# Performance work log

Hardware: AMD Instinct MI355X
Metric: run time of the kernel (lower is better)

## Reference

```python
import jax, jax.numpy as jnp
import numpy as np
import math

B, T, C, D = 8, 2048, 1024, 1024
N_LAYER, LAYER_ID = 24, 12


def setup_inputs() -> dict:
    key = jax.random.key(0)
    ks = jax.random.split(key, 5)
    r01 = LAYER_ID / (N_LAYER - 1)
    r10 = 1.0 - LAYER_ID / N_LAYER
    ddd = np.arange(C, dtype=np.float64) / C                      # (C,)
    h = np.arange(D, dtype=np.float64)
    decay_speed = -5 + 8 * (h / (D - 1)) ** (0.7 + 1.3 * r01)     # time_decay init
    zigzag = ((np.arange(D) + 1) % 3 - 1) * 0.5
    time_first = np.log(0.3) + zigzag
    scale = C ** -0.5
    return {
        "x": jax.random.normal(ks[0], (B, T, C), jnp.float32),
        "time_decay": jnp.asarray(decay_speed, jnp.float32),
        "time_first": jnp.asarray(time_first, jnp.float32),
        "time_mix_k": jnp.asarray(ddd ** r10, jnp.float32),
        "time_mix_v": jnp.asarray(ddd ** r10 + 0.3 * r01, jnp.float32),
        "time_mix_r": jnp.asarray(ddd ** (0.5 * r10), jnp.float32),
        "Wk": jax.random.normal(ks[1], (D, C), jnp.float32) * scale,
        "Wv": jax.random.normal(ks[2], (D, C), jnp.float32) * scale,
        "Wr": jax.random.normal(ks[3], (D, C), jnp.float32) * scale,
        "Wo": jax.random.normal(ks[4], (C, D), jnp.float32) * scale,
    }


def _wkv(time_decay, time_first, k, v):
    # wkv_t = (e^{u+k_t} v_t + A_{t-1}) / (e^{u+k_t} + B_{t-1})
    # A_t = e^w A_{t-1} + e^{k_t} v_t ;  B_t likewise with v=1 ;  w = -exp(time_decay)
    # Exactly the math of the original conv1d-with-exp-curve trick, in O(T).
    ew = jnp.exp(-jnp.exp(time_decay))   # (D,)
    eu = jnp.exp(time_first)             # (D,)
    ek = jnp.exp(k)                      # [B,T,D]
    ekv = ek * v

    def step(carry, inp):
        a, b = carry                     # [B,D] each
        ekt, ekvt = inp                  # [B,D] each
        out = (eu * ekvt + a) / (eu * ekt + b)
        return (ew * a + ekvt, ew * b + ekt), out

    init = (jnp.zeros_like(ek[:, 0]), jnp.zeros_like(ek[:, 0]))
    xs = (jnp.swapaxes(ek, 0, 1), jnp.swapaxes(ekv, 0, 1))  # [T,B,D]
    _, out = jax.lax.scan(step, init, xs)
    return jnp.swapaxes(out, 0, 1)       # [B,T,D]


def reference(x, time_decay, time_first, time_mix_k, time_mix_v, time_mix_r, Wk, Wv, Wr, Wo):
    # time_shift: prepend zero row, drop last (ZeroPad2d((0,0,1,-1)))
    xx = jnp.pad(x, ((0, 0), (1, 0), (0, 0)))[:, :-1]
    xk = x * time_mix_k + xx * (1 - time_mix_k)
    xv = x * time_mix_v + xx * (1 - time_mix_v)
    xr = x * time_mix_r + xx * (1 - time_mix_r)
    k = jnp.einsum('btc,dc->btd', xk, Wk)
    v = jnp.einsum('btc,dc->btd', xv, Wv)
    sr = jax.nn.sigmoid(jnp.einsum('btc,dc->btd', xr, Wr))
    rwkv = sr * _wkv(time_decay, time_first, k, v)
    return jnp.einsum('btd,cd->btc', rwkv, Wo)
```

## Files before the change

### kernel.cpp

```cpp
#include <hip/hip_runtime.h>
#include <cstdint>
#include <cstddef>

#define Bb 8
#define Tt 2048
#define Cc 1024
#define Dd 1024
#define Mm (Bb*Tt)
#define CL 64
#define NCH (Tt/CL)


typedef __bf16  bf16x8  __attribute__((ext_vector_type(8)));
typedef float   floatx4 __attribute__((ext_vector_type(4)));

#define MFMA16(a, b, c) __builtin_amdgcn_mfma_f32_16x16x32_bf16((a), (b), (c), 0, 0, 0)

__device__ __forceinline__ ushort f2bf(float f) {
    unsigned u = __float_as_uint(f);
    u = (u + 0x7FFF + ((u >> 16) & 1)) >> 16;
    return (ushort)u;
}
__device__ __forceinline__ float bf2f(ushort u) {
    return __uint_as_float(((unsigned)u) << 16);
}

__device__ __forceinline__ void load_lds16(const void* g, void* l) {
    __builtin_amdgcn_global_load_lds((__attribute__((address_space(1))) void*)(g),
                                     (__attribute__((address_space(3))) void*)(l),
                                     16, 0, 0);
}

#define CFENCE asm volatile("" ::: "memory")
#define BARRIER do { CFENCE; __builtin_amdgcn_s_barrier(); CFENCE; } while (0)

__global__ __launch_bounds__(256) void prep_mix3(
        const float* __restrict__ x,
        const float* __restrict__ mk, const float* __restrict__ mv,
        const float* __restrict__ mr,
        ushort* __restrict__ xk, ushort* __restrict__ xv, ushort* __restrict__ xr) {
    int i  = blockIdx.x * 256 + threadIdx.x;
    int cq = i & (Cc / 8 - 1);
    int m  = i >> 7;
    int t  = m & (Tt - 1);
    float xc[8], xp[8];
    *(float4*)&xc[0] = ((const float4*)x)[i * 2];
    *(float4*)&xc[4] = ((const float4*)x)[i * 2 + 1];
    if (t != 0) {
        *(float4*)&xp[0] = ((const float4*)x)[(i - Cc / 8) * 2];
        *(float4*)&xp[4] = ((const float4*)x)[(i - Cc / 8) * 2 + 1];
    } else {
#pragma unroll
        for (int j = 0; j < 8; j++) xp[j] = 0.f;
    }
    float wk[8], wv[8], wr[8];
    *(float4*)&wk[0] = ((const float4*)mk)[cq * 2];
    *(float4*)&wk[4] = ((const float4*)mk)[cq * 2 + 1];
    *(float4*)&wv[0] = ((const float4*)mv)[cq * 2];
    *(float4*)&wv[4] = ((const float4*)mv)[cq * 2 + 1];
    *(float4*)&wr[0] = ((const float4*)mr)[cq * 2];
    *(float4*)&wr[4] = ((const float4*)mr)[cq * 2 + 1];
    ushort ok[8], ov[8], orr[8];
#pragma unroll
    for (int j = 0; j < 8; j++) {
        float d = xc[j] - xp[j];
        ok[j]  = f2bf(xp[j] + d * wk[j]);
        ov[j]  = f2bf(xp[j] + d * wv[j]);
        orr[j] = f2bf(xp[j] + d * wr[j]);
    }
    ((ulonglong2*)xk)[i] = *(const ulonglong2*)ok;
    ((ulonglong2*)xv)[i] = *(const ulonglong2*)ov;
    ((ulonglong2*)xr)[i] = *(const ulonglong2*)orr;
}

__global__ __launch_bounds__(256) void cvt_w(
        const float* __restrict__ wk, const float* __restrict__ wv,
        const float* __restrict__ wr, const float* __restrict__ wo,
        ushort* __restrict__ ok, ushort* __restrict__ ov,
        ushort* __restrict__ orr, ushort* __restrict__ oo) {
    int i = blockIdx.x * 256 + threadIdx.x;
    int sel = i >> 18;
    int j = i & ((1 << 18) - 1);
    const float* s = sel == 0 ? wk : sel == 1 ? wv : sel == 2 ? wr : wo;
    ushort* d      = sel == 0 ? ok : sel == 1 ? ov : sel == 2 ? orr : oo;
    float4 f = ((const float4*)s)[j];
    ushort4 o;
    o.x = f2bf(f.x); o.y = f2bf(f.y); o.z = f2bf(f.z); o.w = f2bf(f.w);
    ((ushort4*)d)[j] = o;
}

struct Gemm9 {
    floatx4 acc[8][4];
    int quad, fr, wm, wn;

    __device__ __forceinline__ void run(
            const ushort* __restrict__ A, const ushort* __restrict__ Bw,
            long tm, long tn, int Kdim, __bf16* LDSb) {
        const int tid  = threadIdx.x;
        const int lane = tid & 63;
        quad = lane >> 4;
        fr   = lane & 15;
        const int wave = tid >> 6;
        wm = (wave >> 2) * 128;
        wn = (wave & 3) * 64;
        const int x7 = fr & 7;
        const int g0 = (quad ^ x7) * 8;
        const int g1 = ((4 + quad) ^ x7) * 8;

        const int srow = tid >> 3;
        const int scol = ((tid & 7) ^ (srow & 7)) * 8;
        const int wlds = wave * 512;
        const ushort* Ag[4];
#pragma unroll
        for (int j = 0; j < 4; j++)
            Ag[j] = A + (tm + j * 64 + srow) * (long)Kdim + scol;

        auto stageA = [&](int buf, long koff) {
            __bf16* d = LDSb + buf * 16384;
#pragma unroll
            for (int j = 0; j < 4; j++)
                load_lds16(Ag[j] + koff, d + j * 4096 + wlds);
        };

        const ushort* Bq[4];
#pragma unroll
        for (int ni = 0; ni < 4; ni++)
            Bq[ni] = Bw + (tn + wn + ni * 16 + fr) * (long)Kdim + quad * 8;

        floatx4 zero = {0.f, 0.f, 0.f, 0.f};
#pragma unroll
        for (int ai = 0; ai < 8; ai++)
#pragma unroll
            for (int nj = 0; nj < 4; nj++) acc[ai][nj] = zero;

        const int NT = Kdim >> 6;

        stageA(0, 0);
        CFENCE;
        if (NT > 1) stageA(1, 64);
        bf16x8 b0[4], b1[4], bn0[4];
#pragma unroll
        for (int ni = 0; ni < 4; ni++) b0[ni] = *(const bf16x8*)(Bq[ni]);
#pragma unroll
        for (int ni = 0; ni < 4; ni++) b1[ni] = *(const bf16x8*)(Bq[ni] + 32);
        asm volatile("s_waitcnt vmcnt(12)" ::: "memory");
        BARRIER;

        int bc = 0, bs = 2;
        for (int T = 0; T < NT; ++T) {
            const __bf16* Ab = LDSb + bc * 16384;
            const long knext = (long)(T + 1) * 64;
            if (T + 1 < NT) {
#pragma unroll
                for (int ni = 0; ni < 4; ni++)
                    bn0[ni] = *(const bf16x8*)(Bq[ni] + knext);
            }
            if (T + 2 < NT)
                stageA(bs, (long)(T + 2) * 64);

            bf16x8 a0[4], a1[4];
#pragma unroll
            for (int r = 0; r < 4; r++)
                a0[r] = *(const bf16x8*)&Ab[(wm + r * 16 + fr) * 64 + g0];
#pragma unroll
            for (int r = 0; r < 4; r++)
                a1[r] = *(const bf16x8*)&Ab[(wm + 64 + r * 16 + fr) * 64 + g0];
            __builtin_amdgcn_s_setprio(1);
#pragma unroll
            for (int r = 0; r < 4; r++)
#pragma unroll
                for (int ni = 0; ni < 4; ni++)
                    acc[r][ni] = MFMA16(a0[r], b0[ni], acc[r][ni]);
#pragma unroll
            for (int r = 0; r < 4; r++)
#pragma unroll
                for (int ni = 0; ni < 4; ni++)
                    acc[4 + r][ni] = MFMA16(a1[r], b0[ni], acc[4 + r][ni]);
            __builtin_amdgcn_s_setprio(0);
#pragma unroll
            for (int r = 0; r < 4; r++)
                a0[r] = *(const bf16x8*)&Ab[(wm + r * 16 + fr) * 64 + g1];
#pragma unroll
            for (int r = 0; r < 4; r++)
                a1[r] = *(const bf16x8*)&Ab[(wm + 64 + r * 16 + fr) * 64 + g1];
            __builtin_amdgcn_s_setprio(1);
#pragma unroll
            for (int r = 0; r < 4; r++)
#pragma unroll
                for (int ni = 0; ni < 4; ni++)
                    acc[r][ni] = MFMA16(a0[r], b1[ni], acc[r][ni]);
#pragma unroll
            for (int r = 0; r < 4; r++)
#pragma unroll
                for (int ni = 0; ni < 4; ni++)
                    acc[4 + r][ni] = MFMA16(a1[r], b1[ni], acc[4 + r][ni]);
            __builtin_amdgcn_s_setprio(0);

            if (T + 1 < NT) {
#pragma unroll
                for (int ni = 0; ni < 4; ni++)
                    b1[ni] = *(const bf16x8*)(Bq[ni] + knext + 32);
#pragma unroll
                for (int ni = 0; ni < 4; ni++) b0[ni] = bn0[ni];
                asm volatile("s_waitcnt vmcnt(8)" ::: "memory");
                BARRIER;
            }
            if (++bc == 3) bc = 0;
            if (++bs == 3) bs = 0;
        }
    }
};

template<int MODE>
__global__ __launch_bounds__(512, 2) void gemm_nt(
        const ushort* __restrict__ A, const ushort* __restrict__ Bw,
        void* __restrict__ Co, int Ndim, int Kdim) {
    __shared__ __attribute__((aligned(16))) __bf16 LDSb[3 * 16384];
    const int orig = blockIdx.y * 64 + blockIdx.x;
    const int L    = (orig & 7) * 32 + (orig >> 3);
    const long tm = (long)(L >> 2) * 256;
    const long tn = (long)(L & 3) * 256;
    Gemm9 g;
    g.run(A, Bw, tm, tn, Kdim, LDSb);
#pragma unroll
    for (int ai = 0; ai < 8; ai++)
#pragma unroll
        for (int nj = 0; nj < 4; nj++)
#pragma unroll
            for (int r = 0; r < 4; r++) {
                long grow = tm + g.wm + ai * 16 + g.quad * 4 + r;
                long gcol = tn + g.wn + nj * 16 + g.fr;
                float v = g.acc[ai][nj][r];
                if (MODE == 2) v = 1.f / (1.f + __expf(-v));
                if (MODE == 0)      ((float*)Co)[grow * Ndim + gcol] = v;
                else if (MODE == 3) ((_Float16*)Co)[grow * Ndim + gcol] = (_Float16)v;
                else                ((ushort*)Co)[grow * Ndim + gcol] = f2bf(v);
            }
}

__global__ __launch_bounds__(512, 2) void gemm3_nt(
        const ushort* __restrict__ xk, const ushort* __restrict__ xv,
        const ushort* __restrict__ xr,
        const ushort* __restrict__ wk, const ushort* __restrict__ wv,
        const ushort* __restrict__ wr,
        _Float16* __restrict__ kb, ushort* __restrict__ vb,
        ushort* __restrict__ sb) {
    __shared__ __attribute__((aligned(16))) __bf16 LDSb[3 * 16384];
    const int orig = blockIdx.y * 64 + blockIdx.x;
    const int L    = (orig & 7) * 96 + (orig >> 3);
    const int proj = L >> 8;
    const int rem  = L & 255;
    const long tm = (long)(rem >> 2) * 256;
    const long tn = (long)(rem & 3) * 256;
    const ushort* A  = proj == 0 ? xk : proj == 1 ? xv : xr;
    const ushort* Bw = proj == 0 ? wk : proj == 1 ? wv : wr;
    Gemm9 g;
    g.run(A, Bw, tm, tn, Cc, LDSb);
#pragma unroll
    for (int ai = 0; ai < 8; ai++)
#pragma unroll
        for (int nj = 0; nj < 4; nj++)
#pragma unroll
            for (int r = 0; r < 4; r++) {
                long grow = tm + g.wm + ai * 16 + g.quad * 4 + r;
                long gcol = tn + g.wn + nj * 16 + g.fr;
                long off = grow * Dd + gcol;
                float v = g.acc[ai][nj][r];
                if (proj == 0)      kb[off] = (_Float16)v;
                else if (proj == 1) vb[off] = f2bf(v);
                else                sb[off] = f2bf(1.f / (1.f + __expf(-v)));
            }
}

__global__ __launch_bounds__(256) void wkv_part(
        const _Float16* __restrict__ kb, const ushort* __restrict__ vb,
        const float* __restrict__ decay,
        float* __restrict__ pa, float* __restrict__ pb) {
    int gid = blockIdx.x * 256 + threadIdx.x;
    int d = gid & (Dd - 1);
    int c = (gid >> 10) & (NCH - 1);
    int b = gid >> 15;
    float ew = __expf(-__expf(decay[d]));
    size_t base = ((size_t)b * Tt + (size_t)c * CL) * Dd + d;
    float a = 0.f, bs = 0.f;
    for (int i0 = 0; i0 < CL; i0 += 8) {
        float kr[8], vr[8];
#pragma unroll
        for (int j = 0; j < 8; j++) {
            size_t idx = base + (size_t)(i0 + j) * Dd;
            kr[j] = (float)kb[idx]; vr[j] = bf2f(vb[idx]);
        }
#pragma unroll
        for (int j = 0; j < 8; j++) {
            float ek = __expf(kr[j]);
            a  = ew * a  + ek * vr[j];
            bs = ew * bs + ek;
        }
    }
    int sidx = c * (Bb * Dd) + b * Dd + d;
    pa[sidx] = a; pb[sidx] = bs;
}

__global__ __launch_bounds__(256) void wkv_prefix(
        const float* __restrict__ pa, const float* __restrict__ pb,
        const float* __restrict__ decay,
        float* __restrict__ sa, float* __restrict__ sb) {
    int gid = blockIdx.x * 256 + threadIdx.x;
    int d = gid & (Dd - 1);
    float ewL = __expf(-__expf(decay[d]) * (float)CL);
    float ca = 0.f, cb = 0.f;
#pragma unroll
    for (int c = 0; c < NCH; c++) {
        int idx = c * (Bb * Dd) + gid;
        sa[idx] = ca; sb[idx] = cb;
        ca = ewL * ca + pa[idx];
        cb = ewL * cb + pb[idx];
    }
}

__global__ __launch_bounds__(256) void wkv_chunk(
        const _Float16* __restrict__ kb, const ushort* __restrict__ vb,
        const ushort* __restrict__ sr,
        const float* __restrict__ decay, const float* __restrict__ tf,
        const float* __restrict__ sa, const float* __restrict__ sb,
        ushort* __restrict__ rw) {
    int gid = blockIdx.x * 256 + threadIdx.x;
    int d = gid & (Dd - 1);
    int c = (gid >> 10) & (NCH - 1);
    int b = gid >> 15;
    float ew = __expf(-__expf(decay[d]));
    float eu = __expf(tf[d]);
    int sidx = c * (Bb * Dd) + b * Dd + d;
    float a = sa[sidx], bs = sb[sidx];
    size_t base = ((size_t)b * Tt + (size_t)c * CL) * Dd + d;
    for (int i0 = 0; i0 < CL; i0 += 8) {
        float kr[8], vr[8], rr[8];
#pragma unroll
        for (int j = 0; j < 8; j++) {
            size_t idx = base + (size_t)(i0 + j) * Dd;
            kr[j] = (float)kb[idx]; vr[j] = bf2f(vb[idx]); rr[j] = bf2f(sr[idx]);
        }
#pragma unroll
        for (int j = 0; j < 8; j++) {
            float ek  = __expf(kr[j]);
            float ekv = ek * vr[j];
            float out = (eu * ekv + a) / (eu * ek + bs);
            a  = ew * a  + ekv;
            bs = ew * bs + ek;
            rw[base + (size_t)(i0 + j) * Dd] = f2bf(rr[j] * out);
        }
    }
}

extern "C" void kernel_launch(void* const* d_in, const int* in_sizes, int n_in,
                              void* d_out, int out_size, void* d_ws, size_t ws_size,
                              hipStream_t stream) {
    (void)in_sizes; (void)n_in; (void)out_size;
    const float* x  = (const float*)d_in[0];
    const float* td = (const float*)d_in[1];
    const float* tf = (const float*)d_in[2];
    const float* mk = (const float*)d_in[3];
    const float* mv = (const float*)d_in[4];
    const float* mr = (const float*)d_in[5];
    const float* Wk = (const float*)d_in[6];
    const float* Wv = (const float*)d_in[7];
    const float* Wr = (const float*)d_in[8];
    const float* Wo = (const float*)d_in[9];
    float* out = (float*)d_out;

    const size_t xsz = (size_t)Mm * Cc * 2;
    const size_t wsz = (size_t)Dd * Cc * 2;
    const size_t ssz = (size_t)Bb * NCH * Dd * 4;
    const size_t need_merged = 6 * xsz + 4 * wsz + 4 * ssz;

    char* p = (char*)d_ws;
    auto take = [&](size_t n) { char* r = p; p += n; return r; };
    ushort*   xk = (ushort*)take(xsz);
    ushort*   xv = (ushort*)take(xsz);
    ushort*   xr = (ushort*)take(xsz);
    _Float16* kb = (_Float16*)take(xsz);
    const bool merged = ws_size >= need_merged;
    ushort *vb, *sb, *rw;
    if (merged) {
        vb = (ushort*)take(xsz);
        sb = (ushort*)take(xsz);
        rw = xk;
    } else {
        vb = xk;
        sb = xv;
        rw = xr;
    }
    ushort* wk = (ushort*)take(wsz);
    ushort* wv = (ushort*)take(wsz);
    ushort* wr = (ushort*)take(wsz);
    ushort* wo = (ushort*)take(wsz);
    float*  pa = (float*)take(ssz);
    float*  pb = (float*)take(ssz);
    float*  sa = (float*)take(ssz);
    float*  sbst = (float*)take(ssz);

    dim3 g1(Mm / 256, Dd / 256);
    dim3 g2(Mm / 256, Cc / 256);
    dim3 g3(Mm / 256, 3 * Dd / 256);
    const int wkv_grid = (Bb * NCH * Dd) / 256;

    cvt_w<<<4096, 256, 0, stream>>>(Wk, Wv, Wr, Wo, wk, wv, wr, wo);
    prep_mix3<<<Mm * Cc / 8 / 256, 256, 0, stream>>>(x, mk, mv, mr, xk, xv, xr);

    if (merged) {
        gemm3_nt<<<g3, 512, 0, stream>>>(xk, xv, xr, wk, wv, wr, kb, vb, sb);
    } else {
        gemm_nt<3><<<g1, 512, 0, stream>>>(xk, wk, kb, Dd, Cc);
        gemm_nt<1><<<g1, 512, 0, stream>>>(xv, wv, vb, Dd, Cc);
        gemm_nt<2><<<g1, 512, 0, stream>>>(xr, wr, sb, Dd, Cc);
    }

    wkv_part  <<<wkv_grid, 256, 0, stream>>>(kb, vb, td, pa, pb);
    wkv_prefix<<<(Bb * Dd) / 256, 256, 0, stream>>>(pa, pb, td, sa, sbst);
    wkv_chunk <<<wkv_grid, 256, 0, stream>>>(kb, vb, sb, td, tf, sa, sbst, rw);

    gemm_nt<0><<<g2, 512, 0, stream>>>(rw, wo, out, Cc, Dd);
}
```

Before: 403.0 us.

## Stage both GEMM operands through LDS with 32-wide K tiles and split-phase MFMA

The shared GEMM core now stages both the activation and the weight tiles into LDS using K-steps of 32 and a triple buffer, where before only the activation tile went through LDS and the weights were read per lane straight from global memory. Each K-step is split into two MFMA halves, with prefetch of the next A and B tiles placed between them and extra barriers around each half. This targets the uncoalesced, redundant global loads of the weight operand and lowers register pressure. In exchange it doubles the number of K iterations and adds several barriers per iteration, which could reduce MFMA issue density.

```diff
diff --git a/kernel.cpp b/kernel.cpp
--- a/kernel.cpp
+++ b/kernel.cpp
@@ -89,7 +89,7 @@
     ((ushort4*)d)[j] = o;
 }
 
-struct Gemm9 {
+struct GemmR10 {
     floatx4 acc[8][4];
     int quad, fr, wm, wn;
 
@@ -103,29 +103,26 @@
         const int wave = tid >> 6;
         wm = (wave >> 2) * 128;
         wn = (wave & 3) * 64;
-        const int x7 = fr & 7;
-        const int g0 = (quad ^ x7) * 8;
-        const int g1 = ((4 + quad) ^ x7) * 8;
-
-        const int srow = tid >> 3;
-        const int scol = ((tid & 7) ^ (srow & 7)) * 8;
+        const int goff = (quad ^ ((fr >> 1) & 3)) * 8;
+
+        const int srow = tid >> 2;
+        const int scol = ((tid & 3) ^ ((tid >> 3) & 3)) * 8;
         const int wlds = wave * 512;
-        const ushort* Ag[4];
-#pragma unroll
-        for (int j = 0; j < 4; j++)
-            Ag[j] = A + (tm + j * 64 + srow) * (long)Kdim + scol;
-
-        auto stageA = [&](int buf, long koff) {
+        const ushort* Ag0 = A  + (tm + srow) * (long)Kdim + scol;
+        const ushort* Ag1 = Ag0 + 128 * (long)Kdim;
+        const ushort* Bg0 = Bw + (tn + srow) * (long)Kdim + scol;
+        const ushort* Bg1 = Bg0 + 128 * (long)Kdim;
+
+        auto stageA = [&](int buf, long ko) {
             __bf16* d = LDSb + buf * 16384;
-#pragma unroll
-            for (int j = 0; j < 4; j++)
-                load_lds16(Ag[j] + koff, d + j * 4096 + wlds);
+            load_lds16(Ag0 + ko, d + wlds);
+            load_lds16(Ag1 + ko, d + 4096 + wlds);
         };
-
-        const ushort* Bq[4];
-#pragma unroll
-        for (int ni = 0; ni < 4; ni++)
-            Bq[ni] = Bw + (tn + wn + ni * 16 + fr) * (long)Kdim + quad * 8;
+        auto stageB = [&](int buf, long ko) {
+            __bf16* d = LDSb + buf * 16384 + 8192;
+            load_lds16(Bg0 + ko, d + wlds);
+            load_lds16(Bg1 + ko, d + 4096 + wlds);
+        };
 
         floatx4 zero = {0.f, 0.f, 0.f, 0.f};
 #pragma unroll
@@ -133,80 +130,56 @@
 #pragma unroll
             for (int nj = 0; nj < 4; nj++) acc[ai][nj] = zero;
 
-        const int NT = Kdim >> 6;
-
-        stageA(0, 0);
-        CFENCE;
-        if (NT > 1) stageA(1, 64);
-        bf16x8 b0[4], b1[4], bn0[4];
-#pragma unroll
-        for (int ni = 0; ni < 4; ni++) b0[ni] = *(const bf16x8*)(Bq[ni]);
-#pragma unroll
-        for (int ni = 0; ni < 4; ni++) b1[ni] = *(const bf16x8*)(Bq[ni] + 32);
-        asm volatile("s_waitcnt vmcnt(12)" ::: "memory");
+        const int NT = Kdim >> 5;
+
+        stageA(0, 0);  stageB(0, 0);
+        stageA(1, 32); stageB(1, 32);
+        asm volatile("s_waitcnt vmcnt(4)" ::: "memory");
         BARRIER;
 
-        int bc = 0, bs = 2;
+        int bc = 0;
         for (int T = 0; T < NT; ++T) {
             const __bf16* Ab = LDSb + bc * 16384;
-            const long knext = (long)(T + 1) * 64;
+            const __bf16* Bbf = Ab + 8192;
+            const int sb = (bc + 2 >= 3) ? bc - 1 : bc + 2;
+            const bool pf = (T + 2 < NT);
+            const long ko = (long)(T + 2) * 32;
+
+            bf16x8 a[8], b0, b1, b2, b3;
+#pragma unroll
+            for (int i = 0; i < 8; i++)
+                a[i] = *(const bf16x8*)&Ab[(wm + i * 16 + fr) * 32 + goff];
+            b0 = *(const bf16x8*)&Bbf[(wn + fr) * 32 + goff];
+            b1 = *(const bf16x8*)&Bbf[(wn + 16 + fr) * 32 + goff];
+            if (pf) stageA(sb, ko);
+            BARRIER;
+            __builtin_amdgcn_s_setprio(1);
+#pragma unroll
+            for (int i = 0; i < 8; i++) {
+                acc[i][0] = MFMA16(a[i], b0, acc[i][0]);
+                acc[i][1] = MFMA16(a[i], b1, acc[i][1]);
+            }
+            __builtin_amdgcn_s_setprio(0);
+            BARRIER;
+
+            b2 = *(const bf16x8*)&Bbf[(wn + 32 + fr) * 32 + goff];
+            b3 = *(const bf16x8*)&Bbf[(wn + 48 + fr) * 32 + goff];
+            if (pf) stageB(sb, ko);
             if (T + 1 < NT) {
-#pragma unroll
-                for (int ni = 0; ni < 4; ni++)
-                    bn0[ni] = *(const bf16x8*)(Bq[ni] + knext);
-            }
-            if (T + 2 < NT)
-                stageA(bs, (long)(T + 2) * 64);
-
-            bf16x8 a0[4], a1[4];
-#pragma unroll
-            for (int r = 0; r < 4; r++)
-                a0[r] = *(const bf16x8*)&Ab[(wm + r * 16 + fr) * 64 + g0];
-#pragma unroll
-            for (int r = 0; r < 4; r++)
-                a1[r] = *(const bf16x8*)&Ab[(wm + 64 + r * 16 + fr) * 64 + g0];
+                if (pf) asm volatile("s_waitcnt vmcnt(4)" ::: "memory");
+                else    asm volatile("s_waitcnt vmcnt(0)" ::: "memory");
+            }
+            BARRIER;
             __builtin_amdgcn_s_setprio(1);
 #pragma unroll
-            for (int r = 0; r < 4; r++)
-#pragma unroll
-                for (int ni = 0; ni < 4; ni++)
-                    acc[r][ni] = MFMA16(a0[r], b0[ni], acc[r][ni]);
-#pragma unroll
-            for (int r = 0; r < 4; r++)
-#pragma unroll
-                for (int ni = 0; ni < 4; ni++)
-                    acc[4 + r][ni] = MFMA16(a1[r], b0[ni], acc[4 + r][ni]);
+            for (int i = 0; i < 8; i++) {
+                acc[i][2] = MFMA16(a[i], b2, acc[i][2]);
+                acc[i][3] = MFMA16(a[i], b3, acc[i][3]);
+            }
             __builtin_amdgcn_s_setprio(0);
-#pragma unroll
-            for (int r = 0; r < 4; r++)
-                a0[r] = *(const bf16x8*)&Ab[(wm + r * 16 + fr) * 64 + g1];
-#pragma unroll
-            for (int r = 0; r < 4; r++)
-                a1[r] = *(const bf16x8*)&Ab[(wm + 64 + r * 16 + fr) * 64 + g1];
-            __builtin_amdgcn_s_setprio(1);
-#pragma unroll
-            for (int r = 0; r < 4; r++)
-#pragma unroll
-                for (int ni = 0; ni < 4; ni++)
-                    acc[r][ni] = MFMA16(a0[r], b1[ni], acc[r][ni]);
-#pragma unroll
-            for (int r = 0; r < 4; r++)
-#pragma unroll
-                for (int ni = 0; ni < 4; ni++)
-                    acc[4 + r][ni] = MFMA16(a1[r], b1[ni], acc[4 + r][ni]);
-            __builtin_amdgcn_s_setprio(0);
-
-            if (T + 1 < NT) {
-#pragma unroll
-                for (int ni = 0; ni < 4; ni++)
-                    b1[ni] = *(const bf16x8*)(Bq[ni] + knext + 32);
-#pragma unroll
-                for (int ni = 0; ni < 4; ni++) b0[ni] = bn0[ni];
-                asm volatile("s_waitcnt vmcnt(8)" ::: "memory");
-                BARRIER;
-            }
-            if (++bc == 3) bc = 0;
-            if (++bs == 3) bs = 0;
+            BARRIER;
+
+            bc = (bc + 1 == 3) ? 0 : bc + 1;
         }
     }
 };
@@ -220,7 +193,7 @@
     const int L    = (orig & 7) * 32 + (orig >> 3);
     const long tm = (long)(L >> 2) * 256;
     const long tn = (long)(L & 3) * 256;
-    Gemm9 g;
+    GemmR10 g;
     g.run(A, Bw, tm, tn, Kdim, LDSb);
 #pragma unroll
     for (int ai = 0; ai < 8; ai++)
@@ -254,7 +227,7 @@
     const long tn = (long)(rem & 3) * 256;
     const ushort* A  = proj == 0 ? xk : proj == 1 ? xv : xr;
     const ushort* Bw = proj == 0 ? wk : proj == 1 ? wv : wr;
-    Gemm9 g;
+    GemmR10 g;
     g.run(A, Bw, tm, tn, Cc, LDSb);
 #pragma unroll
     for (int ai = 0; ai < 8; ai++)
```

Measured after the change: 376.0 us. 6.7% less time.
